# Kernel optimization log

Hardware: AMD Instinct MI355X
Metric: run time of the kernel (lower is better)

Reference implementation:

```python
import jax, jax.numpy as jnp
import numpy as np

# Interval [A, B] with B < inf -> hidden_dim = B, steps = B - A + 1 (TemporalOperator.__init__)
A = 0
B = 63
HIDDEN = B            # hidden_dim
STEPS = B - A + 1     # window length of the reduction
T = 4096              # time dimension
D = 8192              # state dimension


def setup_inputs() -> dict:
    key = jax.random.key(0)
    signal = jax.random.normal(key, (T, D), dtype=jnp.float32)
    return {"signal": signal}


def reference(signal):
    # subformula = identity, so trace == signal.
    # _initialize_hidden_state: h0 = ones([hidden_dim, ...]) * signal[:1]
    h0 = jnp.broadcast_to(signal[0], (HIDDEN,) + signal.shape[1:])

    def step(h, x):
        # x: [D], h: [HIDDEN, D]
        # _cell (finite-interval branch):
        #   hidden_state_ = M @ h + b * x  == shift h up by one, append x at the end
        #   input_ = concat([h, x])[:steps]; output = min(input_, dim=0)  (Always operator)
        hx = jnp.concatenate([h, x[None]], axis=0)       # [HIDDEN+1, D]
        out = jnp.min(hx[:STEPS], axis=0)                # [D]
        h_new = jnp.concatenate([h[1:], x[None]], axis=0)  # M @ h + b * x
        return h_new, out

    _, outputs = jax.lax.scan(step, h0, signal)          # outputs: [T, D]
    return outputs
```

## Files before the change

### kernel.cpp

```cpp
#include <hip/hip_runtime.h>
#include <cmath>


constexpr int T_DIM = 4096;
constexpr int D_DIM = 8192;
constexpr int W = 64;
constexpr int TSEG = 128;
constexpr int NB = TSEG / W;
constexpr int CHUNK = 16;
constexpr int THREADS = 256;

__global__ __launch_bounds__(THREADS, 2)
void TemporalOperator_74182675136668_kernel(const float* __restrict__ in,
                                            float* __restrict__ out) {
    const int col = blockIdx.x * THREADS + threadIdx.x;
    const int t0 = blockIdx.y * TSEG;
    const float* pin = in + col;
    float* pout = out + col;

    float A[W];

    if (t0 == 0) {
#pragma unroll
        for (int i = 0; i < W; ++i) A[i] = INFINITY;
    } else {
#pragma unroll
        for (int i = 0; i < W; ++i) A[i] = pin[(t0 - W + i) * D_DIM];
#pragma unroll
        for (int i = W - 2; i >= 0; --i) A[i] = fminf(A[i], A[i + 1]);
    }

#pragma unroll
    for (int b = 0; b < NB; ++b) {
        const int tb = t0 + b * W;
        float L = INFINITY;
#pragma unroll
        for (int c = 0; c < W / CHUNK; ++c) {
            float X[CHUNK];
#pragma unroll
            for (int j = 0; j < CHUNK; ++j)
                X[j] = pin[(tb + c * CHUNK + j) * D_DIM];
#pragma unroll
            for (int j = 0; j < CHUNK; ++j) {
                const int i = c * CHUNK + j;
                L = fminf(L, X[j]);
                const float o = (i + 1 < W) ? fminf(L, A[i + 1]) : L;
                __builtin_nontemporal_store(o, &pout[(tb + i) * D_DIM]);
                A[i] = X[j];
            }
        }
#pragma unroll
        for (int i = W - 2; i >= 0; --i) A[i] = fminf(A[i], A[i + 1]);
    }
}

extern "C" void kernel_launch(void* const* d_in, const int* in_sizes, int n_in,
                              void* d_out, int out_size, void* d_ws, size_t ws_size,
                              hipStream_t stream) {
    const float* in = (const float*)d_in[0];
    float* out = (float*)d_out;
    dim3 grid(D_DIM / THREADS, T_DIM / TSEG);
    TemporalOperator_74182675136668_kernel<<<grid, THREADS, 0, stream>>>(in, out);
}
```

Baseline: 242.4 us.

## Move window suffix-min state to LDS and double-buffer input chunk loads

Moves the 64-entry per-thread suffix-min array from registers into shared memory, indexed per thread. This frees registers so the loop over T blocks no longer needs full unrolling. It adds double-buffered prefetch of the next 16-row input chunk so global loads overlap the min/store work. The time segment per block doubles, which halves the redundant halo reads but also halves the grid's parallelism along T. LDS traffic replaces register access and may cost latency.

After: 237.2 us. 2.1% less time.

```diff
diff --git a/kernel.cpp b/kernel.cpp
--- a/kernel.cpp
+++ b/kernel.cpp
@@ -1,56 +1,94 @@
 #include <hip/hip_runtime.h>
 #include <cmath>
+#include <utility>
 
 
 constexpr int T_DIM = 4096;
 constexpr int D_DIM = 8192;
 constexpr int W = 64;
-constexpr int TSEG = 128;
+constexpr int TSEG = 256;
 constexpr int NB = TSEG / W;
 constexpr int CHUNK = 16;
+constexpr int NCH = W / CHUNK;
 constexpr int THREADS = 256;
+
+template <class F, int... Is>
+__device__ __forceinline__ void unroll_seq(F&& f, std::integer_sequence<int, Is...>) {
+    (f(std::integral_constant<int, Is>{}), ...);
+}
+template <int N, class F>
+__device__ __forceinline__ void unroll(F&& f) {
+    unroll_seq(static_cast<F&&>(f), std::make_integer_sequence<int, N>{});
+}
 
 __global__ __launch_bounds__(THREADS, 2)
 void TemporalOperator_74182675136668_kernel(const float* __restrict__ in,
                                             float* __restrict__ out) {
-    const int col = blockIdx.x * THREADS + threadIdx.x;
+    __shared__ float S[W][THREADS];
+
+    const int tid = threadIdx.x;
+    const int col = blockIdx.x * THREADS + tid;
     const int t0 = blockIdx.y * TSEG;
     const float* pin = in + col;
     float* pout = out + col;
 
-    float A[W];
+    float X[CHUNK], Y[CHUNK];
 
     if (t0 == 0) {
 #pragma unroll
-        for (int i = 0; i < W; ++i) A[i] = INFINITY;
+        for (int i = 0; i < W; ++i) S[i][tid] = INFINITY;
     } else {
+        const float* pp = pin + (t0 - W) * D_DIM;
+        unroll<CHUNK>([&](auto J) { X[J] = pp[J * D_DIM]; });
 #pragma unroll
-        for (int i = 0; i < W; ++i) A[i] = pin[(t0 - W + i) * D_DIM];
+        for (int c = 0; c < NCH; ++c) {
+            if (c + 1 < NCH)
+                unroll<CHUNK>([&](auto J) { Y[J] = pp[((c + 1) * CHUNK + J) * D_DIM]; });
+            unroll<CHUNK>([&](auto J) { S[c * CHUNK + J][tid] = X[J]; });
+            if (c + 1 < NCH)
+                unroll<CHUNK>([&](auto J) { X[J] = Y[J]; });
+        }
+        float s = S[W - 1][tid];
 #pragma unroll
-        for (int i = W - 2; i >= 0; --i) A[i] = fminf(A[i], A[i + 1]);
+        for (int i = W - 2; i >= 0; --i) {
+            float x = S[i][tid];
+            s = fminf(x, s);
+            S[i][tid] = s;
+        }
     }
 
-#pragma unroll
+    unroll<CHUNK>([&](auto J) { X[J] = pin[(t0 + J) * D_DIM]; });
+
     for (int b = 0; b < NB; ++b) {
         const int tb = t0 + b * W;
         float L = INFINITY;
 #pragma unroll
-        for (int c = 0; c < W / CHUNK; ++c) {
-            float X[CHUNK];
-#pragma unroll
-            for (int j = 0; j < CHUNK; ++j)
-                X[j] = pin[(tb + c * CHUNK + j) * D_DIM];
-#pragma unroll
-            for (int j = 0; j < CHUNK; ++j) {
+        for (int c = 0; c < NCH; ++c) {
+            const bool pf = (b * W + (c + 1) * CHUNK < TSEG);
+            if (pf)
+                unroll<CHUNK>([&](auto J) {
+                    Y[J] = pin[(tb + (c + 1) * CHUNK + J) * D_DIM];
+                });
+            unroll<CHUNK>([&](auto J) {
+                constexpr int j = J;
                 const int i = c * CHUNK + j;
                 L = fminf(L, X[j]);
-                const float o = (i + 1 < W) ? fminf(L, A[i + 1]) : L;
+                const float o = (i + 1 < W) ? fminf(L, S[i + 1][tid]) : L;
                 __builtin_nontemporal_store(o, &pout[(tb + i) * D_DIM]);
-                A[i] = X[j];
+                S[i][tid] = X[j];
+            });
+            if (pf)
+                unroll<CHUNK>([&](auto J) { X[J] = Y[J]; });
+        }
+        if (b + 1 < NB) {
+            float s = S[W - 1][tid];
+#pragma unroll
+            for (int i = W - 2; i >= 0; --i) {
+                float x = S[i][tid];
+                s = fminf(x, s);
+                S[i][tid] = s;
             }
         }
-#pragma unroll
-        for (int i = W - 2; i >= 0; --i) A[i] = fminf(A[i], A[i + 1]);
     }
 }
 
```
